# Kernel optimization log

Hardware: AMD Instinct MI355X
Metric: run time of the kernel (lower is better)

## Reference

```python
import jax, jax.numpy as jnp
import numpy as np

DEPTH = 8            # 2**DEPTH - 1 = 255 internal nodes, 2**DEPTH = 256 leaves
BATCH = 2048
NUM_CLASSES = 200
EPS = 1e-07


def setup_inputs() -> dict:
    key = jax.random.key(0)
    k_sim, k_leaf = jax.random.split(key)
    # similarities[i] is the LOG prob of routing right at internal node i
    # (heap order: children of i are 2i+1, 2i+2). Log-probs are <= 0.
    sims = -(jax.random.uniform(k_sim, (2 ** DEPTH - 1, BATCH), dtype=jnp.float32) * 3.0 + 0.01)
    leaf_logits = jax.random.normal(k_leaf, (2 ** DEPTH, NUM_CLASSES), dtype=jnp.float32)
    return {"similarities": sims, "leaf_logits": leaf_logits}


def reference(similarities, leaf_logits):
    B = similarities.shape[1]
    C = leaf_logits.shape[1]
    log2 = jnp.asarray(np.log(2.0), dtype=similarities.dtype)
    # Leaf log-distributions, broadcast over batch: [n_leaves, B, C]
    dists = jnp.broadcast_to(jax.nn.log_softmax(leaf_logits, axis=-1)[:, None, :],
                             (leaf_logits.shape[0], B, C))
    # Bottom-up over tree levels (fixed small loop over DEPTH levels).
    for level in reversed(range(DEPTH)):
        n = 2 ** level
        p_right = similarities[n - 1: 2 * n - 1][:, :, None]   # [n, B, 1]
        a = jnp.abs(p_right) + EPS
        # numerically-stable log(1 - exp(-a)), split at log(2) as in the source
        p_left = jnp.where(a < log2,
                           jnp.log(-jnp.expm1(-a)),
                           jnp.log1p(-jnp.exp(-a)))
        # children of level-l node j are the consecutive pair (2j, 2j+1) in level l+1
        dists = jnp.logaddexp(p_left + dists[0::2], p_right + dists[1::2])  # [n, B, C]
    return dists[0]  # root pred_logits: [B, C]
```

## Files before the change

### kernel.cpp

```cpp
#include <hip/hip_runtime.h>

#define DEPTH 8
#define NINT 255
#define NLEAF 256
#define BATCH 2048
#define NCLS 200
#define EPS 1e-7f
#define TB 8
#define LPAD 264
#define NTILE 13

typedef float f32x4 __attribute__((ext_vector_type(4)));
typedef __bf16 bf16x8 __attribute__((ext_vector_type(8)));
typedef unsigned short u16x8 __attribute__((ext_vector_type(8)));

static __device__ __forceinline__ unsigned short f2bf(float f) {
    unsigned int u = __builtin_bit_cast(unsigned int, f);
    return (unsigned short)((u + 0x8000u) >> 16);
}

__global__ __launch_bounds__(64) void leaf_softmax(
    const float* __restrict__ logits, unsigned short* __restrict__ Et) {
    const int l = blockIdx.x;
    const int lane = threadIdx.x;
    const float* row = logits + l * NCLS;

    float e[4];
    float Z = 0.f;
#pragma unroll
    for (int j = 0; j < 4; ++j) {
        const int c = lane + 64 * j;
        e[j] = (c < NCLS) ? __expf(row[c]) : 0.f;
        Z += e[j];
    }
#pragma unroll
    for (int off = 32; off >= 1; off >>= 1)
        Z += __shfl_xor(Z, off);
    const float invZ = __builtin_amdgcn_rcpf(Z);

#pragma unroll
    for (int j = 0; j < 4; ++j) {
        const int c = lane + 64 * j;
        if (c < NCLS) Et[c * NLEAF + l] = f2bf(e[j] * invZ);
    }
    if (lane < 8) Et[(NCLS + lane) * NLEAF + l] = 0;
}

__global__ __launch_bounds__(256) void tree_gemm(
    const float* __restrict__ sims, const unsigned short* __restrict__ Et,
    float* __restrict__ out) {
    __shared__ unsigned short Wt[16 * LPAD];
    __shared__ float pr_s[NINT * TB];
    __shared__ float pl_s[NINT * TB];
    __shared__ float D_s[TB * NCLS];

    const int tid = threadIdx.x;
    const int b0 = blockIdx.x * TB;

    float prv[8];
#pragma unroll
    for (int p = 0; p < 8; ++p) {
        const int idx = tid + 256 * p;
        if (idx < NINT * TB)
            prv[p] = sims[(idx >> 3) * BATCH + b0 + (idx & 7)];
    }

    const int lane = tid & 63;
    const int wave = tid >> 6;
    const int mn = lane & 15;
    const int quad = lane >> 4;
    const int t0 = wave, t1 = wave + 4, t2 = wave + 8, t3 = wave + 12;

    const bf16x8 pb0 = *(const bf16x8*)(Et + (t0 * 16 + mn) * NLEAF + quad * 8);
    const bf16x8 pb1 = *(const bf16x8*)(Et + (t1 * 16 + mn) * NLEAF + quad * 8);
    const bf16x8 pb2 = *(const bf16x8*)(Et + (t2 * 16 + mn) * NLEAF + quad * 8);
    const bf16x8 pb3 = *(const bf16x8*)(Et + (t3 * 16 + mn) * NLEAF * (t3 < NTILE) + quad * 8);

    {
        unsigned int* wz = (unsigned int*)(Wt + 8 * LPAD);
        for (int i = tid; i < (8 * LPAD) / 2; i += 256) wz[i] = 0u;
    }

#pragma unroll
    for (int p = 0; p < 8; ++p) {
        const int idx = tid + 256 * p;
        if (idx < NINT * TB) {
            const float pr = prv[p];
            const float pl = __logf(1.0f - __expf(pr - EPS));
            pr_s[idx] = pr;
            pl_s[idx] = pl;
        }
    }
    __syncthreads();

    {
        const int q = tid >> 3;
        const int b = tid & 7;
        const int a = 31 + q;

        float s5 = 0.f;
        int n = a;
#pragma unroll
        for (int d = 0; d < 5; ++d) {
            const int par = (n - 1) >> 1;
            s5 += ((n & 1) == 0) ? pr_s[par * TB + b] : pl_s[par * TB + b];
            n = par;
        }
        const float c60 = s5 + pl_s[a * TB + b];
        const float c61 = s5 + pr_s[a * TB + b];
        const int n60 = 2 * a + 1, n61 = 2 * a + 2;
        const float c7[4] = { c60 + pl_s[n60 * TB + b], c60 + pr_s[n60 * TB + b],
                              c61 + pl_s[n61 * TB + b], c61 + pr_s[n61 * TB + b] };
        u16x8 wrow;
#pragma unroll
        for (int i = 0; i < 8; ++i) {
            const int j7 = i >> 1;
            const int p7 = 127 + 4 * q + j7;
            const float w = c7[j7] + ((i & 1) ? pr_s[p7 * TB + b]
                                              : pl_s[p7 * TB + b]);
            wrow[i] = f2bf(__expf(w));
        }
        *(u16x8*)(Wt + b * LPAD + 8 * q) = wrow;
    }
    __syncthreads();

    f32x4 acc0 = {0.f, 0.f, 0.f, 0.f};
    f32x4 acc1 = {0.f, 0.f, 0.f, 0.f};
    f32x4 acc2 = {0.f, 0.f, 0.f, 0.f};
    f32x4 acc3 = {0.f, 0.f, 0.f, 0.f};

#pragma unroll
    for (int s = 0; s < 8; ++s) {
        const int ko = s * 32 + quad * 8;
        const bf16x8 a = *(const bf16x8*)(Wt + mn * LPAD + ko);
        const bf16x8 bv0 = (s == 0) ? pb0
                         : *(const bf16x8*)(Et + (t0 * 16 + mn) * NLEAF + ko);
        acc0 = __builtin_amdgcn_mfma_f32_16x16x32_bf16(a, bv0, acc0, 0, 0, 0);
        const bf16x8 bv1 = (s == 0) ? pb1
                         : *(const bf16x8*)(Et + (t1 * 16 + mn) * NLEAF + ko);
        acc1 = __builtin_amdgcn_mfma_f32_16x16x32_bf16(a, bv1, acc1, 0, 0, 0);
        const bf16x8 bv2 = (s == 0) ? pb2
                         : *(const bf16x8*)(Et + (t2 * 16 + mn) * NLEAF + ko);
        acc2 = __builtin_amdgcn_mfma_f32_16x16x32_bf16(a, bv2, acc2, 0, 0, 0);
        if (wave == 0) {
            const bf16x8 bv3 = (s == 0) ? pb3
                             : *(const bf16x8*)(Et + (t3 * 16 + mn) * NLEAF + ko);
            acc3 = __builtin_amdgcn_mfma_f32_16x16x32_bf16(a, bv3, acc3, 0, 0, 0);
        }
    }

    if (quad < 2) {
#pragma unroll
        for (int i = 0; i < 4; ++i) {
            const int t = (i == 0) ? t0 : (i == 1) ? t1 : (i == 2) ? t2 : t3;
            if (t >= NTILE) continue;
            const f32x4 acc = (i == 0) ? acc0 : (i == 1) ? acc1
                            : (i == 2) ? acc2 : acc3;
            const int c = t * 16 + mn;
            if (c < NCLS) {
#pragma unroll
                for (int r = 0; r < 4; ++r)
                    D_s[(quad * 4 + r) * NCLS + c] = acc[r];
            }
        }
    }
    __syncthreads();
    {
        f32x4* po = (f32x4*)(out + (size_t)b0 * NCLS);
        const f32x4* ps = (const f32x4*)D_s;
#pragma unroll
        for (int it = 0; it < 2; ++it) {
            const int idx = tid + 256 * it;
            if (idx < (TB * NCLS) / 4) {
                f32x4 v = ps[idx];
                v[0] = __logf(v[0]); v[1] = __logf(v[1]);
                v[2] = __logf(v[2]); v[3] = __logf(v[3]);
                po[idx] = v;
            }
        }
    }
}

extern "C" void kernel_launch(void* const* d_in, const int* in_sizes, int n_in,
                              void* d_out, int out_size, void* d_ws, size_t ws_size,
                              hipStream_t stream) {
    const float* sims = (const float*)d_in[0];
    const float* logits = (const float*)d_in[1];
    float* out = (float*)d_out;
    unsigned short* Et = (unsigned short*)d_ws;

    leaf_softmax<<<NLEAF, 64, 0, stream>>>(logits, Et);
    tree_gemm<<<BATCH / TB, 256, 0, stream>>>(sims, Et, out);
}
```

Before: 65.81 us.

## Fuse leaf softmax into tree GEMM kernel via cooperative grid sync

```diff
diff --git a/kernel.cpp b/kernel.cpp
--- a/kernel.cpp
+++ b/kernel.cpp
@@ -1,4 +1,7 @@
 #include <hip/hip_runtime.h>
+#include <hip/hip_cooperative_groups.h>
+
+namespace cg = cooperative_groups;
 
 #define DEPTH 8
 #define NINT 255
@@ -19,44 +22,20 @@
     return (unsigned short)((u + 0x8000u) >> 16);
 }
 
-__global__ __launch_bounds__(64) void leaf_softmax(
-    const float* __restrict__ logits, unsigned short* __restrict__ Et) {
-    const int l = blockIdx.x;
-    const int lane = threadIdx.x;
-    const float* row = logits + l * NCLS;
-
-    float e[4];
-    float Z = 0.f;
-#pragma unroll
-    for (int j = 0; j < 4; ++j) {
-        const int c = lane + 64 * j;
-        e[j] = (c < NCLS) ? __expf(row[c]) : 0.f;
-        Z += e[j];
-    }
-#pragma unroll
-    for (int off = 32; off >= 1; off >>= 1)
-        Z += __shfl_xor(Z, off);
-    const float invZ = __builtin_amdgcn_rcpf(Z);
-
-#pragma unroll
-    for (int j = 0; j < 4; ++j) {
-        const int c = lane + 64 * j;
-        if (c < NCLS) Et[c * NLEAF + l] = f2bf(e[j] * invZ);
-    }
-    if (lane < 8) Et[(NCLS + lane) * NLEAF + l] = 0;
-}
-
-__global__ __launch_bounds__(256) void tree_gemm(
-    const float* __restrict__ sims, const unsigned short* __restrict__ Et,
-    float* __restrict__ out) {
+__global__ __launch_bounds__(256) void tree_fused(
+    const float* __restrict__ sims, const float* __restrict__ logits,
+    unsigned short* __restrict__ Et, float* __restrict__ out) {
     __shared__ unsigned short Wt[16 * LPAD];
     __shared__ float pr_s[NINT * TB];
     __shared__ float pl_s[NINT * TB];
     __shared__ float D_s[TB * NCLS];
+    __shared__ float Zp[4];
 
     const int tid = threadIdx.x;
+    const int l = blockIdx.x;
     const int b0 = blockIdx.x * TB;
 
+    const float lg = (tid < NCLS) ? logits[l * NCLS + tid] : 0.f;
     float prv[8];
 #pragma unroll
     for (int p = 0; p < 8; ++p) {
@@ -67,14 +46,15 @@
 
     const int lane = tid & 63;
     const int wave = tid >> 6;
-    const int mn = lane & 15;
-    const int quad = lane >> 4;
-    const int t0 = wave, t1 = wave + 4, t2 = wave + 8, t3 = wave + 12;
 
-    const bf16x8 pb0 = *(const bf16x8*)(Et + (t0 * 16 + mn) * NLEAF + quad * 8);
-    const bf16x8 pb1 = *(const bf16x8*)(Et + (t1 * 16 + mn) * NLEAF + quad * 8);
-    const bf16x8 pb2 = *(const bf16x8*)(Et + (t2 * 16 + mn) * NLEAF + quad * 8);
-    const bf16x8 pb3 = *(const bf16x8*)(Et + (t3 * 16 + mn) * NLEAF * (t3 < NTILE) + quad * 8);
+    const float ecl = (tid < NCLS) ? __expf(lg) : 0.f;
+    {
+        float z = ecl;
+#pragma unroll
+        for (int off = 32; off >= 1; off >>= 1)
+            z += __shfl_xor(z, off);
+        if (lane == 0) Zp[wave] = z;
+    }
 
     {
         unsigned int* wz = (unsigned int*)(Wt + 8 * LPAD);
@@ -86,12 +66,18 @@
         const int idx = tid + 256 * p;
         if (idx < NINT * TB) {
             const float pr = prv[p];
-            const float pl = __logf(1.0f - __expf(pr - EPS));
             pr_s[idx] = pr;
-            pl_s[idx] = pl;
+            pl_s[idx] = __logf(1.0f - __expf(pr - EPS));
         }
     }
     __syncthreads();
+
+    {
+        const float Z = (Zp[0] + Zp[1]) + (Zp[2] + Zp[3]);
+        const float invZ = __builtin_amdgcn_rcpf(Z);
+        if (tid < NCLS)           Et[tid * NLEAF + l] = f2bf(ecl * invZ);
+        else if (tid < NCLS + 8)  Et[tid * NLEAF + l] = 0;
+    }
 
     {
         const int q = tid >> 3;
@@ -122,7 +108,12 @@
         }
         *(u16x8*)(Wt + b * LPAD + 8 * q) = wrow;
     }
-    __syncthreads();
+
+    cg::this_grid().sync();
+
+    const int mn = lane & 15;
+    const int quad = lane >> 4;
+    const int t0 = wave, t1 = wave + 4, t2 = wave + 8, t3 = wave + 12;
 
     f32x4 acc0 = {0.f, 0.f, 0.f, 0.f};
     f32x4 acc1 = {0.f, 0.f, 0.f, 0.f};
@@ -133,18 +124,14 @@
     for (int s = 0; s < 8; ++s) {
         const int ko = s * 32 + quad * 8;
         const bf16x8 a = *(const bf16x8*)(Wt + mn * LPAD + ko);
-        const bf16x8 bv0 = (s == 0) ? pb0
-                         : *(const bf16x8*)(Et + (t0 * 16 + mn) * NLEAF + ko);
+        const bf16x8 bv0 = *(const bf16x8*)(Et + (t0 * 16 + mn) * NLEAF + ko);
         acc0 = __builtin_amdgcn_mfma_f32_16x16x32_bf16(a, bv0, acc0, 0, 0, 0);
-        const bf16x8 bv1 = (s == 0) ? pb1
-                         : *(const bf16x8*)(Et + (t1 * 16 + mn) * NLEAF + ko);
+        const bf16x8 bv1 = *(const bf16x8*)(Et + (t1 * 16 + mn) * NLEAF + ko);
         acc1 = __builtin_amdgcn_mfma_f32_16x16x32_bf16(a, bv1, acc1, 0, 0, 0);
-        const bf16x8 bv2 = (s == 0) ? pb2
-                         : *(const bf16x8*)(Et + (t2 * 16 + mn) * NLEAF + ko);
+        const bf16x8 bv2 = *(const bf16x8*)(Et + (t2 * 16 + mn) * NLEAF + ko);
         acc2 = __builtin_amdgcn_mfma_f32_16x16x32_bf16(a, bv2, acc2, 0, 0, 0);
         if (wave == 0) {
-            const bf16x8 bv3 = (s == 0) ? pb3
-                             : *(const bf16x8*)(Et + (t3 * 16 + mn) * NLEAF + ko);
+            const bf16x8 bv3 = *(const bf16x8*)(Et + (t3 * 16 + mn) * NLEAF + ko);
             acc3 = __builtin_amdgcn_mfma_f32_16x16x32_bf16(a, bv3, acc3, 0, 0, 0);
         }
     }
@@ -189,6 +176,7 @@
     float* out = (float*)d_out;
     unsigned short* Et = (unsigned short*)d_ws;
 
-    leaf_softmax<<<NLEAF, 64, 0, stream>>>(logits, Et);
-    tree_gemm<<<BATCH / TB, 256, 0, stream>>>(sims, Et, out);
+    void* args[] = { (void*)&sims, (void*)&logits, (void*)&Et, (void*)&out };
+    hipLaunchCooperativeKernel((const void*)tree_fused, dim3(BATCH / TB),
+                               dim3(256), args, 0, stream);
 }
```

New measurement: 106.0 us. 1.61x slower.
